# Kernel tuning notes

Measured on AMD Instinct MI355X. Metric: run time of the kernel, lower is better.

## Reference

```python
import jax, jax.numpy as jnp
import numpy as np

N = 4096        # num_of_drugs / nodes
EMB = 256       # emb_size
ATT = 128       # atten_size
H = 3           # nheads
PAIRS = 131072  # scored drug pairs
ALPHA = 0.2     # LeakyReLU slope in GraphAttentionLayer
NEG = -9e15     # pyGAT mask value


def setup_inputs() -> dict:
    key = jax.random.key(0)
    ks = jax.random.split(key, 14)
    s = 0.05
    return dict(
        a_idx=jax.random.randint(ks[0], (PAIRS,), 0, N),
        b_idx=jax.random.randint(ks[1], (PAIRS,), 0, N),
        adj=jax.random.randint(ks[2], (N, N), 0, 2).astype(jnp.int32),
        emb=jax.random.normal(ks[3], (N, EMB)) * s,          # nn.Embedding table
        emb_b=jax.random.normal(ks[4], (N, 1)) * s,          # bias embedding table
        W1=jax.random.normal(ks[5], (H, EMB, ATT)) * s,      # layer-1 head weights
        av1=jax.random.normal(ks[6], (H, 2 * ATT, 1)) * s,   # layer-1 attn vectors
        W2=jax.random.normal(ks[7], (H, H * ATT, ATT)) * s,  # layer-2 head weights
        av2=jax.random.normal(ks[8], (H, 2 * ATT, 1)) * s,   # layer-2 attn vectors
        a_mix=jax.random.normal(ks[9], (1, 1)),              # self.a
        b_mix=jax.random.normal(ks[10], (1, 1)),             # self.b
        lin_W=jax.random.normal(ks[11], (H * ATT, ATT)) * s,
        lin_b=jnp.zeros((ATT,)),
        out_W=jax.random.normal(ks[12], (ATT + 1, 1)) * s,
        out_b=jnp.zeros((1,)),
    )


def _gat_head(h, W, av, mask):
    # standard pyGAT dense GraphAttentionLayer (eval mode, concat=True)
    Wh = h @ W                                   # [N, F]
    f = Wh.shape[1]
    e = jax.nn.leaky_relu(Wh @ av[:f] + (Wh @ av[f:]).T, ALPHA)  # [N, N]
    e = jnp.where(mask, e, NEG)
    att = jax.nn.softmax(e, axis=1)
    return jax.nn.elu(att @ Wh)                  # [N, F]


def _gat_multi(h, Ws, avs, mask):
    outs = jax.vmap(lambda W, av: _gat_head(h, W, av, mask))(Ws, avs)  # [H, N, F]
    Hn, Nn, Fn = outs.shape
    return jnp.transpose(outs, (1, 0, 2)).reshape(Nn, Hn * Fn)  # cat over heads, dim=1


def reference(a_idx, b_idx, adj, emb, emb_b, W1, av1, W2, av2,
              a_mix, b_mix, lin_W, lin_b, out_W, out_b):
    mask = adj > 0
    at1 = _gat_multi(emb, W1, av1, mask)   # [N, H*ATT]
    at2 = _gat_multi(at1, W2, av2, mask)   # [N, H*ATT]
    denom = a_mix + b_mix
    atten = at1 * (a_mix / denom) + at2 * (b_mix / denom)
    x = atten[a_idx] * atten[b_idx]        # index_select + elementwise mul
    x = jax.nn.gelu(x @ lin_W + lin_b, approximate=False)
    b_add = jax.nn.gelu(emb_b[a_idx] + emb_b[b_idx], approximate=False)
    x = jnp.concatenate([x, b_add], axis=1)
    return jax.nn.sigmoid(x @ out_W + out_b)  # [PAIRS, 1]
```

## Files before the change

### kernel.cpp

```cpp
#include <hip/hip_runtime.h>

typedef unsigned long long u64;
typedef unsigned short u16;
typedef __bf16 bf16_t;
typedef bf16_t bf16x8 __attribute__((ext_vector_type(8)));
typedef _Float16 f16_t;
typedef f16_t f16x8 __attribute__((ext_vector_type(8)));
typedef f16_t f16x2 __attribute__((ext_vector_type(2)));
typedef __fp16 h16n_t;
typedef h16n_t h16n2 __attribute__((ext_vector_type(2)));
typedef float f32x4 __attribute__((ext_vector_type(4)));
typedef float f32x2 __attribute__((ext_vector_type(2)));

#define NN 4096
#define NH 3
#define NPAIR 131072
#define LOG2E 1.4426950408889634f

#if __has_builtin(__builtin_amdgcn_cvt_pk_fp8_f32) && \
    __has_builtin(__builtin_amdgcn_cvt_pk_f32_fp8)
#define HAVE_FP8_CVT 1
#else
#define HAVE_FP8_CVT 0
#endif

union U8 { uint4 u; bf16x8 b; };
union UH { uint4 u; f16x8 h; };
union UH2 { f16x2 h; unsigned int u; };
union UHN2 { h16n2 h; unsigned int u; };

__device__ __forceinline__ u16 f2us(float f) {
  unsigned int x = __float_as_uint(f);
  x = x + 0x7fffu + ((x >> 16) & 1u);
  return (u16)(x >> 16);
}
__device__ __forceinline__ float us2f(u16 u) {
  return __uint_as_float(((unsigned int)u) << 16);
}
__device__ __forceinline__ unsigned int pk2(float a, float b) {
  return (unsigned int)f2us(a) | ((unsigned int)f2us(b) << 16);
}
__device__ __forceinline__ unsigned int pkh2(float a, float b) {
#if __has_builtin(__builtin_amdgcn_cvt_pkrtz)
  UHN2 cv;
  cv.h = __builtin_amdgcn_cvt_pkrtz(a, b);
  return cv.u;
#else
  UH2 cv;
  cv.h[0] = (f16_t)a;
  cv.h[1] = (f16_t)b;
  return cv.u;
#endif
}
__device__ __forceinline__ u16 f2h16(float a) {
  UH2 cv;
  cv.h[0] = (f16_t)a;
  cv.h[1] = (f16_t)0.f;
  return (u16)(cv.u & 0xffffu);
}
__device__ __forceinline__ f16x2 h2max(f16x2 a, f16x2 b) {
  f16x2 r;
  r[0] = a[0] > b[0] ? a[0] : b[0];
  r[1] = a[1] > b[1] ? a[1] : b[1];
  return r;
}
__device__ __forceinline__ float exp2fast(float x) {
#if __has_builtin(__builtin_amdgcn_exp2f)
  return __builtin_amdgcn_exp2f(x);
#else
  return __expf(x * 0.6931471805599453f);
#endif
}
__device__ __forceinline__ float erf_fast(float x) {
  float ax = fabsf(x);
  float t = 1.f / fmaf(0.3275911f, ax, 1.f);
  float poly =
      t * (0.254829592f +
           t * (-0.284496736f +
                t * (1.421413741f +
                     t * (-1.453152027f + t * 1.061405429f))));
  float e = exp2fast(-ax * ax * LOG2E);
  float r = 1.f - poly * e;
  return x < 0.f ? -r : r;
}
__device__ __forceinline__ float geluf(float x) {
  return 0.5f * x * (1.f + erf_fast(x * 0.70710678118654752f));
}
__device__ __forceinline__ void gl_lds16(const u16* g, u16* s) {
  __builtin_amdgcn_global_load_lds(
      (const __attribute__((address_space(1))) unsigned int*)g,
      (__attribute__((address_space(3))) unsigned int*)s, 16, 0, 0);
}

#if !HAVE_FP8_CVT
__device__ __forceinline__ float e4m3_f(unsigned int b) {
  unsigned int s = b >> 7, e = (b >> 3) & 15, m = b & 7;
  float v = (e == 0) ? (float)m * 0.001953125f
                     : __uint_as_float(((e + 120u) << 23) | (m << 20));
  return s ? -v : v;
}
__device__ __forceinline__ unsigned int f_e4m3(float f) {
  unsigned int sign = (__float_as_uint(f) >> 24) & 0x80u;
  float a = fabsf(f);
  if (!(a >= 9.765625e-4f)) return sign;
  a = fminf(a, 448.f);
  int e;
  float fr = frexpf(a, &e);
  if (e >= -5) {
    int M = (int)(fr * 16.f + 0.5f);
    int E = e + 6;
    if (M == 16) { M = 8; E += 1; }
    if (E > 15) { E = 15; M = 15; }
    return sign | (unsigned)(E << 3) | (unsigned)(M - 8);
  }
  int M = (int)(a * 512.f + 0.5f);
  if (M > 7) M = 7;
  return sign | (unsigned)M;
}
#endif

__device__ __forceinline__ void dec8lo(uint4 u, float* o) {
#if HAVE_FP8_CVT
  f32x2 p0 = __builtin_amdgcn_cvt_pk_f32_fp8((int)u.x, false);
  f32x2 p1 = __builtin_amdgcn_cvt_pk_f32_fp8((int)u.x, true);
  f32x2 p2 = __builtin_amdgcn_cvt_pk_f32_fp8((int)u.y, false);
  f32x2 p3 = __builtin_amdgcn_cvt_pk_f32_fp8((int)u.y, true);
  o[0] = p0[0]; o[1] = p0[1]; o[2] = p1[0]; o[3] = p1[1];
  o[4] = p2[0]; o[5] = p2[1]; o[6] = p3[0]; o[7] = p3[1];
#else
#pragma unroll
  for (int e = 0; e < 4; ++e) o[e] = e4m3_f((u.x >> (8 * e)) & 0xffu);
#pragma unroll
  for (int e = 0; e < 4; ++e) o[4 + e] = e4m3_f((u.y >> (8 * e)) & 0xffu);
#endif
}
__device__ __forceinline__ void dec8hi(uint4 u, float* o) {
#if HAVE_FP8_CVT
  f32x2 p0 = __builtin_amdgcn_cvt_pk_f32_fp8((int)u.z, false);
  f32x2 p1 = __builtin_amdgcn_cvt_pk_f32_fp8((int)u.z, true);
  f32x2 p2 = __builtin_amdgcn_cvt_pk_f32_fp8((int)u.w, false);
  f32x2 p3 = __builtin_amdgcn_cvt_pk_f32_fp8((int)u.w, true);
  o[0] = p0[0]; o[1] = p0[1]; o[2] = p1[0]; o[3] = p1[1];
  o[4] = p2[0]; o[5] = p2[1]; o[6] = p3[0]; o[7] = p3[1];
#else
#pragma unroll
  for (int e = 0; e < 4; ++e) o[e] = e4m3_f((u.z >> (8 * e)) & 0xffu);
#pragma unroll
  for (int e = 0; e < 4; ++e) o[4 + e] = e4m3_f((u.w >> (8 * e)) & 0xffu);
#endif
}

__global__ __launch_bounds__(256) void k_bitmask(const int* __restrict__ adj,
                                                 u64* __restrict__ bm) {
  int i = blockIdx.x;
  int lane = threadIdx.x & 63;
  int wv = threadIdx.x >> 6;
  const int* row = adj + (size_t)i * NN;
  for (int wq = wv; wq < NN / 64; wq += 4) {
    u64 b = __ballot(row[wq * 64 + lane] > 0);
    if (lane == 0) bm[(size_t)i * (NN / 64) + wq] = b;
  }
}

__global__ __launch_bounds__(256) void k_maskf(const u64* __restrict__ bm,
                                               unsigned int* __restrict__ bmF) {
  int idx = blockIdx.x * 256 + threadIdx.x;
  int l = idx & 63, jc = (idx >> 6) & 127, ib = idx >> 13;
  int li = l & 15, lg = l >> 4;
  const unsigned char* b8 = (const unsigned char*)bm;
  unsigned int v = 0;
#pragma unroll
  for (int m = 0; m < 4; ++m)
    v |= (unsigned int)b8[(size_t)(ib * 64 + m * 16 + li) * 512 + jc * 4 + lg]
         << (8 * m);
  bmF[idx] = v;
}

__global__ __launch_bounds__(256) void k_prep(
    const float* __restrict__ emb, const float* __restrict__ W1,
    const float* __restrict__ W2, const float* __restrict__ linW,
    u16* __restrict__ emb16, u16* __restrict__ WT1, u16* __restrict__ WT2,
    u16* __restrict__ linWT) {
  int idx = blockIdx.x * 256 + threadIdx.x;
  if (idx < 1048576) { emb16[idx] = f2us(emb[idx]); return; }
  idx -= 1048576;
  if (idx < 98304) {
    int h = idx / 32768, r = idx & 32767, f = r >> 8, k = r & 255;
    WT1[idx] = f2us(W1[h * 32768 + k * 128 + f]);
    return;
  }
  idx -= 98304;
  if (idx < 147456) {
    int h = idx / 49152, r = idx % 49152, f = r / 384, k = r % 384;
    WT2[idx] = f2us(W2[h * 49152 + k * 128 + f]);
    return;
  }
  idx -= 147456;
  if (idx < 49152) {
    int f = idx / 384, k = idx % 384;
    linWT[idx] = f2us(linW[k * 128 + f]);
  }
}

template <int K>
__global__ __launch_bounds__(64, 4) void k_wh(const u16* __restrict__ xb,
                                              const u16* __restrict__ WT,
                                              const float* __restrict__ av,
                                              u16* __restrict__ WhTF,
                                              float* __restrict__ E1,
                                              float* __restrict__ F1,
                                              u16* __restrict__ E2h,
                                              u16* __restrict__ F2h) {
  constexpr int NS = K / 32;
  int h = blockIdx.y, l = threadIdx.x, li = l & 15, lg = l >> 4;
  int iw = blockIdx.x * 16;
  const u16* Wb = WT + (size_t)h * 128 * K;
  const u16* xr = xb + (size_t)(iw + li) * K;

  f32x4 acc[8];
#pragma unroll
  for (int nt = 0; nt < 8; ++nt) acc[nt] = (f32x4){0.f, 0.f, 0.f, 0.f};

#pragma unroll 2
  for (int s = 0; s < NS; ++s) {
    int j0 = s * 32 + lg * 8;
    uint4 xa = *(const uint4*)(xr + j0);
    uint4 b[8];
#pragma unroll
    for (int nt = 0; nt < 8; ++nt)
      b[nt] = *(const uint4*)(Wb + (size_t)(nt * 16 + li) * K + j0);
    U8 af;
    af.u = xa;
#pragma unroll
    for (int nt = 0; nt < 8; ++nt) {
      U8 bb;
      bb.u = b[nt];
      acc[nt] = __builtin_amdgcn_mfma_f32_16x16x32_bf16(af.b, bb.b, acc[nt], 0, 0, 0);
    }
  }

  float p1[4] = {0.f, 0.f, 0.f, 0.f}, p2[4] = {0.f, 0.f, 0.f, 0.f};
#pragma unroll
  for (int nt = 0; nt < 8; ++nt) {
    float a1 = av[h * 256 + nt * 16 + li];
    float a2 = av[h * 256 + 128 + nt * 16 + li];
#pragma unroll
    for (int r = 0; r < 4; ++r) {
      p1[r] = fmaf(acc[nt][r], a1, p1[r]);
      p2[r] = fmaf(acc[nt][r], a2, p2[r]);
    }
  }
#pragma unroll
  for (int r = 0; r < 4; ++r) {
#pragma unroll
    for (int o = 1; o < 16; o <<= 1) {
      p1[r] += __shfl_xor(p1[r], o);
      p2[r] += __shfl_xor(p2[r], o);
    }
  }
  if (li == 0) {
#pragma unroll
    for (int r = 0; r < 4; ++r) {
      int idx = h * NN + iw + lg * 4 + r;
      float s1L = p1[r] * LOG2E, s2L = p2[r] * LOG2E;
      E1[idx] = exp2fast(s1L);
      F1[idx] = exp2fast(0.2f * s1L);
      E2h[idx] = f2h16(exp2fast(s2L));
      F2h[idx] = f2h16(exp2fast(0.2f * s2L));
    }
  }
  u16* Wo = WhTF + (size_t)h * 524288;
  int jc = iw >> 5, jin = (iw & 31) + lg * 4;
#pragma unroll
  for (int nt = 0; nt < 8; ++nt) {
    uint2 pw;
    pw.x = pkh2(acc[nt][0], acc[nt][1]);
    pw.y = pkh2(acc[nt][2], acc[nt][3]);
    *(uint2*)(Wo + (size_t)nt * 65536 + (size_t)jc * 512 + li * 32 + jin) = pw;
  }
}

#define WAITC(N)                                                  \
  do {                                                            \
    asm volatile("s_waitcnt vmcnt(" #N ")" ::: "memory");         \
    __builtin_amdgcn_sched_barrier(0);                            \
    __builtin_amdgcn_s_barrier();                                 \
    __builtin_amdgcn_sched_barrier(0);                            \
  } while (0)
#define ROT3(X) X = (X == 2) ? 0 : X + 1

__global__ __launch_bounds__(256, 3) void k_acc(
    const unsigned int* __restrict__ bmF, const u16* __restrict__ WhTF,
    const float* __restrict__ E1, const float* __restrict__ F1,
    const u16* __restrict__ E2h, const u16* __restrict__ F2h,
    u16* __restrict__ Pp, float* __restrict__ dnP) {
  __shared__ __align__(16) u16 Bl[3][4096];
  int h = blockIdx.y, t = threadIdx.x, w = t >> 6, l = t & 63;
  int li = l & 15, lg = l >> 4;
  int rt = blockIdx.x >> 3, kq = blockIdx.x & 7;
  int iw0 = rt * 128 + w * 32;
  int k0 = kq * 512;
  int perm = (l & 15) * 4 + (l >> 4);
  const u16* gsrcA = WhTF + (size_t)h * 524288 + (size_t)w * 65536 +
                     (size_t)(k0 >> 5) * 512 + perm * 8;
  const u16* gsrcB = gsrcA + (size_t)4 * 65536;
  const u16* E2p = E2h + h * NN;
  const u16* F2p = F2h + h * NN;
  f16x2 e1h[2], f1h[2];
#pragma unroll
  for (int mg = 0; mg < 2; ++mg) {
    f16_t e1 = (f16_t)E1[h * NN + iw0 + mg * 16 + li];
    f16_t f1 = (f16_t)F1[h * NN + iw0 + mg * 16 + li];
    e1h[mg][0] = e1; e1h[mg][1] = e1;
    f1h[mg][0] = f1; f1h[mg][1] = f1;
  }
  int mq0 = (iw0 >> 4) & 3;
  const unsigned int* mrow =
      bmF + ((size_t)(iw0 >> 6) * 128 + (k0 >> 5)) * 64 + l;

  f32x4 acc[2][8];
  f32x4 accD[2];
#pragma unroll
  for (int mg = 0; mg < 2; ++mg) {
    accD[mg] = (f32x4){0.f, 0.f, 0.f, 0.f};
#pragma unroll
    for (int nt = 0; nt < 8; ++nt) acc[mg][nt] = (f32x4){0.f, 0.f, 0.f, 0.f};
  }
  UH ones;
  ones.u = make_uint4(0x3C003C00u, 0x3C003C00u, 0x3C003C00u, 0x3C003C00u);

#define STG2(B, S)                                        \
  do {                                                    \
    gl_lds16(gsrcA + (size_t)(S) * 512, &Bl[B][w * 512]); \
    gl_lds16(gsrcB + (size_t)(S) * 512, &Bl[B][(w + 4) * 512]); \
  } while (0)
#define LDSC(SUF, S)                                      \
  do {                                                    \
    int j0_ = k0 + (S) * 32;                              \
    mw##SUF = mrow[(S) * 64];                             \
    Eu##SUF = *(const uint4*)(E2p + j0_ + lg * 8);        \
    Fu##SUF = *(const uint4*)(F2p + j0_ + lg * 8);        \
  } while (0)
#define BODY(SUF)                                                            \
  do {                                                                       \
    unsigned int ew_[4] = {Eu##SUF.x, Eu##SUF.y, Eu##SUF.z, Eu##SUF.w};      \
    unsigned int fw_[4] = {Fu##SUF.x, Fu##SUF.y, Fu##SUF.z, Fu##SUF.w};      \
    UH A_[2];                                                                \
    _Pragma("unroll") for (int mg = 0; mg < 2; ++mg) {                       \
      unsigned int mb_ = (mw##SUF >> (8 * (mq0 + mg))) & 0xffu;              \
      unsigned int aw_[4];                                                   \
      _Pragma("unroll") for (int q = 0; q < 4; ++q) {                        \
        UH2 eh_, fh_, ph_;                                                   \
        eh_.u = ew_[q];                                                      \
        fh_.u = fw_[q];                                                      \
        ph_.h = h2max(e1h[mg] * eh_.h, f1h[mg] * fh_.h);                     \
        unsigned int sel_ = (((mb_ >> (2 * q)) & 1u) ? 0xFFFFu : 0u) |       \
                            (((mb_ >> (2 * q + 1)) & 1u) ? 0xFFFF0000u : 0u);\
        aw_[q] = ph_.u & sel_;                                               \
      }                                                                      \
      A_[mg].u = make_uint4(aw_[0], aw_[1], aw_[2], aw_[3]);                 \
    }                                                                        \
    const u16* bl_ = &Bl[bcur][0] + l * 8;                                   \
    __builtin_amdgcn_s_setprio(1);                                           \
    _Pragma("unroll") for (int nt = 0; nt < 8; ++nt) {                       \
      UH B_;                                                                 \
      B_.u = *(const uint4*)(bl_ + nt * 512);                                \
      acc[0][nt] = __builtin_amdgcn_mfma_f32_16x16x32_f16(A_[0].h, B_.h,     \
                                                  acc[0][nt], 0, 0, 0);      \
      acc[1][nt] = __builtin_amdgcn_mfma_f32_16x16x32_f16(A_[1].h, B_.h,     \
                                                  acc[1][nt], 0, 0, 0);      \
    }                                                                        \
    accD[0] = __builtin_amdgcn_mfma_f32_16x16x32_f16(A_[0].h, ones.h,        \
                                                     accD[0], 0, 0, 0);      \
    accD[1] = __builtin_amdgcn_mfma_f32_16x16x32_f16(A_[1].h, ones.h,        \
                                                     accD[1], 0, 0, 0);      \
    __builtin_amdgcn_s_setprio(0);                                           \
    ROT3(bcur);                                                              \
  } while (0)

  unsigned int mwA, mwB;
  uint4 EuA, FuA, EuB, FuB;
  int bcur = 0, bstg = 2;
  LDSC(A, 0);
  STG2(0, 0);
  STG2(1, 1);
#pragma unroll 1
  for (int s = 0; s < 16; s += 2) {
    WAITC(2);
    LDSC(B, s + 1);
    if (s + 2 < 16) { STG2(bstg, s + 2); ROT3(bstg); }
    BODY(A);
    if (s + 1 == 15) { WAITC(0); } else { WAITC(2); }
    if (s + 2 < 16) LDSC(A, s + 2);
    if (s + 3 < 16) { STG2(bstg, s + 3); ROT3(bstg); }
    BODY(B);
  }
#undef STG2
#undef LDSC
#undef BODY

#pragma unroll
  for (int mg = 0; mg < 2; ++mg) {
    size_t rbase = (size_t)(kq * 3 + h) * NN + iw0 + mg * 16;
#pragma unroll
    for (int nt = 0; nt < 8; ++nt)
#pragma unroll
      for (int r = 0; r < 4; ++r)
        Pp[(rbase + lg * 4 + r) * 128 + nt * 16 + li] = f2us(acc[mg][nt][r]);
    if (li == 0) {
#pragma unroll
      for (int r = 0; r < 4; ++r)
        dnP[rbase + lg * 4 + r] = accD[mg][r];
    }
  }
}

__global__ __launch_bounds__(256) void k_fin(
    const u16* __restrict__ Pp, const float* __restrict__ dnP,
    const float* __restrict__ at1f_in, const float* __restrict__ amix,
    const float* __restrict__ bmix, float* __restrict__ at1f_out,
    u16* __restrict__ at1b_out, unsigned char* __restrict__ att8_out,
    int mode) {
  int gid = blockIdx.x * 256 + threadIdx.x;
  int c4 = gid & 31, row = (gid >> 5) & 4095, h = gid >> 17;
  size_t off = ((size_t)h * NN + row) * 128 + c4 * 4;
  const size_t ks = (size_t)3 * NN * 128;
  float s[4] = {0.f, 0.f, 0.f, 0.f};
  float dsum = 0.f;
#pragma unroll
  for (int q = 0; q < 8; ++q) {
    uint2 v = *(const uint2*)(Pp + q * ks + off);
    s[0] += us2f((u16)(v.x & 0xffffu));
    s[1] += us2f((u16)(v.x >> 16));
    s[2] += us2f((u16)(v.y & 0xffffu));
    s[3] += us2f((u16)(v.y >> 16));
    dsum += dnP[(size_t)(q * 3 + h) * NN + row];
  }
  float inv = 1.f / fmaxf(dsum, 1e-30f);
#pragma unroll
  for (int q = 0; q < 4; ++q) {
    s[q] *= inv;
    s[q] = s[q] > 0.f ? s[q] : (exp2fast(s[q] * LOG2E) - 1.f);
  }
  size_t oi = (size_t)row * 384 + h * 128 + c4 * 4;
  if (mode == 0) {
    *(float4*)(at1f_out + oi) = make_float4(s[0], s[1], s[2], s[3]);
    uint2 pb;
    pb.x = pk2(s[0], s[1]);
    pb.y = pk2(s[2], s[3]);
    *(uint2*)(at1b_out + oi) = pb;
  } else {
    float Am = amix[0], Bm = bmix[0];
    float wa = Am / (Am + Bm), wb = Bm / (Am + Bm);
    float4 a1 = *(const float4*)(at1f_in + oi);
    float m0 = wa * a1.x + wb * s[0];
    float m1 = wa * a1.y + wb * s[1];
    float m2 = wa * a1.z + wb * s[2];
    float m3 = wa * a1.w + wb * s[3];
#if HAVE_FP8_CVT
    int v8 = __builtin_amdgcn_cvt_pk_fp8_f32(m0, m1, 0, false);
    v8 = __builtin_amdgcn_cvt_pk_fp8_f32(m2, m3, v8, true);
#else
    unsigned int v8 = f_e4m3(m0) | (f_e4m3(m1) << 8) | (f_e4m3(m2) << 16) |
                      (f_e4m3(m3) << 24);
#endif
    int gc = h * 128 + c4 * 4;
    int st = gc >> 5, lg2 = (gc >> 3) & 3, e0 = gc & 7;
    int kp = (st >> 1) * 64 + lg2 * 16 + (st & 1) * 8 + e0;
    *(unsigned int*)(att8_out + (size_t)row * 384 + kp) = (unsigned int)v8;
  }
}

__global__ __launch_bounds__(1024) void k_pairs(
    const int* __restrict__ aidx, const int* __restrict__ bidx,
    const unsigned char* __restrict__ att8, const u16* __restrict__ linWT,
    const float* __restrict__ linB, const float* __restrict__ outW,
    const float* __restrict__ outB, const float* __restrict__ embB,
    float* __restrict__ out) {
  __shared__ __align__(16) u16 Wlds[128][392];
  int t = threadIdx.x, w = t >> 6, l = t & 63;
  int li = l & 15, lg = l >> 4;
  {
    int r = t >> 3, seg = (t & 7) * 48;
    const u16* src = linWT + (size_t)r * 384 + seg;
    u16* dst = &Wlds[r][seg];
#pragma unroll
    for (int q = 0; q < 6; ++q)
      *(uint4*)(dst + q * 8) = *(const uint4*)(src + q * 8);
  }
  __syncthreads();

  int p0 = blockIdx.x * 512 + w * 32;
  int ia0 = aidx[p0 + li], ib0 = bidx[p0 + li];
  int ia1 = aidx[p0 + 16 + li], ib1 = bidx[p0 + 16 + li];
  const unsigned char* ra0 = att8 + (size_t)ia0 * 384;
  const unsigned char* rb0 = att8 + (size_t)ib0 * 384;
  const unsigned char* ra1 = att8 + (size_t)ia1 * 384;
  const unsigned char* rb1 = att8 + (size_t)ib1 * 384;
  int boff = lg * 16;

  f32x4 acc[2][8];
#pragma unroll
  for (int g = 0; g < 2; ++g)
#pragma unroll
    for (int nt = 0; nt < 8; ++nt) acc[g][nt] = (f32x4){0.f, 0.f, 0.f, 0.f};

#define LDG8(BUF, S2)                               \
  do {                                              \
    int o_ = (S2) * 64 + boff;                      \
    BUF[0] = *(const uint4*)(ra0 + o_);             \
    BUF[1] = *(const uint4*)(rb0 + o_);             \
    BUF[2] = *(const uint4*)(ra1 + o_);             \
    BUF[3] = *(const uint4*)(rb1 + o_);             \
  } while (0)
#define WORK8(BUF, S2)                                                       \
  do {                                                                       \
    _Pragma("unroll") for (int hf = 0; hf < 2; ++hf) {                       \
      float a0_[8], b0_[8], a1_[8], b1_[8];                                  \
      if (hf == 0) {                                                         \
        dec8lo(BUF[0], a0_); dec8lo(BUF[1], b0_);                            \
        dec8lo(BUF[2], a1_); dec8lo(BUF[3], b1_);                            \
      } else {                                                               \
        dec8hi(BUF[0], a0_); dec8hi(BUF[1], b0_);                            \
        dec8hi(BUF[2], a1_); dec8hi(BUF[3], b1_);                            \
      }                                                                      \
      U8 af0_, af1_;                                                         \
      _Pragma("unroll") for (int e = 0; e < 8; ++e) {                        \
        af0_.b[e] = (bf16_t)(a0_[e] * b0_[e]);                               \
        af1_.b[e] = (bf16_t)(a1_[e] * b1_[e]);                               \
      }                                                                      \
      int j0_ = ((S2) * 2 + hf) * 32 + lg * 8;                               \
      _Pragma("unroll") for (int nt = 0; nt < 8; ++nt) {                     \
        U8 bb_;                                                              \
        bb_.u = *(const uint4*)&Wlds[nt * 16 + li][j0_];                     \
        acc[0][nt] = __builtin_amdgcn_mfma_f32_16x16x32_bf16(af0_.b, bb_.b,  \
                                                    acc[0][nt], 0, 0, 0);    \
        acc[1][nt] = __builtin_amdgcn_mfma_f32_16x16x32_bf16(af1_.b, bb_.b,  \
                                                    acc[1][nt], 0, 0, 0);    \
      }                                                                      \
    }                                                                        \
  } while (0)

  uint4 bX[4], bY[4], bZ[4];
  LDG8(bX, 0);
  LDG8(bY, 1);
  LDG8(bZ, 2);
  WORK8(bX, 0);
  LDG8(bX, 3);
  WORK8(bY, 1);
  LDG8(bY, 4);
  WORK8(bZ, 2);
  LDG8(bZ, 5);
  WORK8(bX, 3);
  WORK8(bY, 4);
  WORK8(bZ, 5);
#undef LDG8
#undef WORK8

#pragma unroll
  for (int g = 0; g < 2; ++g) {
    float z[4] = {0.f, 0.f, 0.f, 0.f};
#pragma unroll
    for (int nt = 0; nt < 8; ++nt) {
      int f = nt * 16 + li;
      float lb = linB[f], ow = outW[f];
#pragma unroll
      for (int r = 0; r < 4; ++r) {
        float y = geluf(acc[g][nt][r] + lb);
        z[r] = fmaf(y, ow, z[r]);
      }
    }
#pragma unroll
    for (int r = 0; r < 4; ++r) {
      z[r] += __shfl_xor(z[r], 1);
      z[r] += __shfl_xor(z[r], 2);
      z[r] += __shfl_xor(z[r], 4);
      z[r] += __shfl_xor(z[r], 8);
    }
    if (li == 0) {
#pragma unroll
      for (int r = 0; r < 4; ++r) {
        int pi = p0 + g * 16 + lg * 4 + r;
        float badd = geluf(embB[aidx[pi]] + embB[bidx[pi]]);
        float zz = z[r] + badd * outW[128] + outB[0];
        out[pi] = 1.f / (1.f + __expf(-zz));
      }
    }
  }
}

extern "C" void kernel_launch(void* const* d_in, const int* in_sizes, int n_in,
                              void* d_out, int out_size, void* d_ws, size_t ws_size,
                              hipStream_t stream) {
  (void)in_sizes; (void)n_in; (void)out_size; (void)ws_size;
  const int* aidx = (const int*)d_in[0];
  const int* bidx = (const int*)d_in[1];
  const int* adj = (const int*)d_in[2];
  const float* emb = (const float*)d_in[3];
  const float* embB = (const float*)d_in[4];
  const float* W1 = (const float*)d_in[5];
  const float* av1 = (const float*)d_in[6];
  const float* W2 = (const float*)d_in[7];
  const float* av2 = (const float*)d_in[8];
  const float* amix = (const float*)d_in[9];
  const float* bmix = (const float*)d_in[10];
  const float* linW = (const float*)d_in[11];
  const float* linB = (const float*)d_in[12];
  const float* outW = (const float*)d_in[13];
  const float* outB = (const float*)d_in[14];

  char* ws = (char*)d_ws;
  u64* bm = (u64*)(ws + 0);
  u16* WhTF = (u16*)(ws + (2u << 20));
  float* E1 = (float*)(ws + (5u << 20));
  float* F1 = (float*)(ws + (5u << 20) + (64u << 10));
  u16* E2h = (u16*)(ws + (5u << 20) + (128u << 10));
  u16* F2h = (u16*)(ws + (5u << 20) + (192u << 10));
  u16* linWT = (u16*)(ws + (5u << 20) + (256u << 10));
  u16* WT1 = (u16*)(ws + (5u << 20) + (384u << 10));
  u16* WT2 = (u16*)(ws + (5u << 20) + (640u << 10));
  float* at1f = (float*)(ws + (6u << 20));
  u16* sh12 = (u16*)(ws + (12u << 20));
  u16* emb16 = sh12;
  u16* at1b = sh12;
  unsigned int* bmF = (unsigned int*)(ws + (15u << 20));
  u16* Pp = (u16*)(ws + (17u << 20));
  float* dnP = (float*)(ws + (41u << 20));
  unsigned char* att8 = (unsigned char*)(ws + (42u << 20));

  k_bitmask<<<NN, 256, 0, stream>>>(adj, bm);
  k_maskf<<<2048, 256, 0, stream>>>(bm, bmF);
  k_prep<<<5248, 256, 0, stream>>>(emb, W1, W2, linW, emb16, WT1, WT2, linWT);
  k_wh<256><<<dim3(256, NH), 64, 0, stream>>>(emb16, WT1, av1, WhTF, E1, F1, E2h, F2h);
  k_acc<<<dim3(256, NH), 256, 0, stream>>>(bmF, WhTF, E1, F1, E2h, F2h, Pp, dnP);
  k_fin<<<1536, 256, 0, stream>>>(Pp, dnP, at1f, amix, bmix, at1f, at1b, att8, 0);
  k_wh<384><<<dim3(256, NH), 64, 0, stream>>>(at1b, WT2, av2, WhTF, E1, F1, E2h, F2h);
  k_acc<<<dim3(256, NH), 256, 0, stream>>>(bmF, WhTF, E1, F1, E2h, F2h, Pp, dnP);
  k_fin<<<1536, 256, 0, stream>>>(Pp, dnP, at1f, amix, bmix, at1f, at1b, att8, 1);
  k_pairs<<<NPAIR / 512, 1024, 0, stream>>>(aidx, bidx, att8, linWT, linB, outW,
                                            outB, embB, (float*)d_out);
}
```

Measured before the change: 155.6 us.

## Fuse adjacency bitmask and MFMA-layout permute; software-pipeline weight loads in k_wh

Merges the two mask kernels into one. Each block ballots a 64x256 tile of adj into shared memory and writes the MFMA-fragment bitmask directly, so the intermediate row-major bitmask no longer goes to global memory and one launch disappears. k_wh now preloads all A fragments and keeps a three-stage register ring of B loads so memory latency overlaps the MFMAs. To make room for the extra registers it lowers the occupancy hint from 4 to 2 waves per SIMD, which could limit latency hiding.

```diff
diff --git a/kernel.cpp b/kernel.cpp
--- a/kernel.cpp
+++ b/kernel.cpp
@@ -150,30 +150,32 @@
 #endif
 }
 
-__global__ __launch_bounds__(256) void k_bitmask(const int* __restrict__ adj,
-                                                 u64* __restrict__ bm) {
-  int i = blockIdx.x;
-  int lane = threadIdx.x & 63;
-  int wv = threadIdx.x >> 6;
-  const int* row = adj + (size_t)i * NN;
-  for (int wq = wv; wq < NN / 64; wq += 4) {
-    u64 b = __ballot(row[wq * 64 + lane] > 0);
-    if (lane == 0) bm[(size_t)i * (NN / 64) + wq] = b;
-  }
-}
-
-__global__ __launch_bounds__(256) void k_maskf(const u64* __restrict__ bm,
-                                               unsigned int* __restrict__ bmF) {
-  int idx = blockIdx.x * 256 + threadIdx.x;
-  int l = idx & 63, jc = (idx >> 6) & 127, ib = idx >> 13;
+__global__ __launch_bounds__(256) void k_mask(const int* __restrict__ adj,
+                                              unsigned int* __restrict__ bmF) {
+  __shared__ __align__(8) unsigned char bml[64][32];
+  int ib = blockIdx.x >> 4, jcg = blockIdx.x & 15;
+  int t = threadIdx.x, w = t >> 6, l = t & 63;
   int li = l & 15, lg = l >> 4;
-  const unsigned char* b8 = (const unsigned char*)bm;
-  unsigned int v = 0;
-#pragma unroll
-  for (int m = 0; m < 4; ++m)
-    v |= (unsigned int)b8[(size_t)(ib * 64 + m * 16 + li) * 512 + jc * 4 + lg]
-         << (8 * m);
-  bmF[idx] = v;
+#pragma unroll 4
+  for (int it = 0; it < 16; ++it) {
+    int r2 = it, row = ib * 64 + w * 16 + r2;
+    const int* src = adj + (size_t)row * NN + jcg * 256;
+#pragma unroll
+    for (int wd = 0; wd < 4; ++wd) {
+      u64 b = __ballot(src[wd * 64 + l] > 0);
+      if (l == 0) *(u64*)&bml[w * 16 + r2][wd * 8] = b;
+    }
+  }
+  __syncthreads();
+#pragma unroll
+  for (int q = 0; q < 2; ++q) {
+    int jj = w * 2 + q;
+    unsigned int v = 0;
+#pragma unroll
+    for (int m = 0; m < 4; ++m)
+      v |= (unsigned int)bml[m * 16 + li][jj * 4 + lg] << (8 * m);
+    bmF[((size_t)ib * 128 + jcg * 8 + jj) * 64 + l] = v;
+  }
 }
 
 __global__ __launch_bounds__(256) void k_prep(
@@ -203,7 +205,7 @@
 }
 
 template <int K>
-__global__ __launch_bounds__(64, 4) void k_wh(const u16* __restrict__ xb,
+__global__ __launch_bounds__(64, 2) void k_wh(const u16* __restrict__ xb,
                                               const u16* __restrict__ WT,
                                               const float* __restrict__ av,
                                               u16* __restrict__ WhTF,
@@ -221,23 +223,36 @@
 #pragma unroll
   for (int nt = 0; nt < 8; ++nt) acc[nt] = (f32x4){0.f, 0.f, 0.f, 0.f};
 
-#pragma unroll 2
+  uint4 xa[NS];
+#pragma unroll
+  for (int s = 0; s < NS; ++s)
+    xa[s] = *(const uint4*)(xr + s * 32 + lg * 8);
+
+  uint4 bbuf[3][8];
+#define LDB(S)                                                               \
+  do {                                                                       \
+    _Pragma("unroll") for (int nt = 0; nt < 8; ++nt)                         \
+        bbuf[(S) % 3][nt] = *(const uint4*)(Wb + (size_t)(nt * 16 + li) * K +\
+                                            (S) * 32 + lg * 8);              \
+  } while (0)
+
+#pragma unroll
+  for (int pf = 0; pf < 3; ++pf) {
+    if (pf < NS) LDB(pf);
+  }
+#pragma unroll
   for (int s = 0; s < NS; ++s) {
-    int j0 = s * 32 + lg * 8;
-    uint4 xa = *(const uint4*)(xr + j0);
-    uint4 b[8];
-#pragma unroll
-    for (int nt = 0; nt < 8; ++nt)
-      b[nt] = *(const uint4*)(Wb + (size_t)(nt * 16 + li) * K + j0);
     U8 af;
-    af.u = xa;
+    af.u = xa[s];
 #pragma unroll
     for (int nt = 0; nt < 8; ++nt) {
       U8 bb;
-      bb.u = b[nt];
+      bb.u = bbuf[s % 3][nt];
       acc[nt] = __builtin_amdgcn_mfma_f32_16x16x32_bf16(af.b, bb.b, acc[nt], 0, 0, 0);
     }
-  }
+    if (s + 3 < NS) LDB(s + 3);
+  }
+#undef LDB
 
   float p1[4] = {0.f, 0.f, 0.f, 0.f}, p2[4] = {0.f, 0.f, 0.f, 0.f};
 #pragma unroll
@@ -610,7 +625,6 @@
   const float* outB = (const float*)d_in[14];
 
   char* ws = (char*)d_ws;
-  u64* bm = (u64*)(ws + 0);
   u16* WhTF = (u16*)(ws + (2u << 20));
   float* E1 = (float*)(ws + (5u << 20));
   float* F1 = (float*)(ws + (5u << 20) + (64u << 10));
@@ -628,8 +642,7 @@
   float* dnP = (float*)(ws + (41u << 20));
   unsigned char* att8 = (unsigned char*)(ws + (42u << 20));
 
-  k_bitmask<<<NN, 256, 0, stream>>>(adj, bm);
-  k_maskf<<<2048, 256, 0, stream>>>(bm, bmF);
+  k_mask<<<1024, 256, 0, stream>>>(adj, bmF);
   k_prep<<<5248, 256, 0, stream>>>(emb, W1, W2, linW, emb16, WT1, WT2, linWT);
   k_wh<256><<<dim3(256, NH), 64, 0, stream>>>(emb16, WT1, av1, WhTF, E1, F1, E2h, F2h);
   k_acc<<<dim3(256, NH), 256, 0, stream>>>(bmF, WhTF, E1, F1, E2h, F2h, Pp, dnP);
```

Result: no change. 154.9 us (-0.5%).
